# Kernel tuning notes

Hardware: AMD Instinct MI355X
Metric: run time of the kernel (lower is better)

The kernel has to match this reference:

```python
import jax, jax.numpy as jnp
import numpy as np

LOG2PI = 1.8378770664093453  # log(2*pi)


def _pixel_positions(d, h, w):
    # centered coordinates, stacked as (x, y, z) per the torch module
    z = jnp.arange(d, dtype=jnp.float32) - (d - 1) / 2.0
    y = jnp.arange(h, dtype=jnp.float32) - (h - 1) / 2.0
    x = jnp.arange(w, dtype=jnp.float32) - (w - 1) / 2.0
    zz = jnp.broadcast_to(z[:, None, None], (d, h, w))
    yy = jnp.broadcast_to(y[None, :, None], (d, h, w))
    xx = jnp.broadcast_to(x[None, None, :], (d, h, w))
    return jnp.stack([xx, yy, zz], axis=-1).reshape(-1, 3)  # (N, 3)


def setup_inputs() -> dict:
    key = jax.random.key(0)
    k0, k1, k2, k3, k4 = jax.random.split(key, 5)
    B, D = 512, 256
    d, h, w = 16, 64, 64
    scale = 1.0 / np.sqrt(D)
    return {
        "representation": jax.random.normal(k0, (B, D), dtype=jnp.float32),
        "mean_w": jax.random.normal(k1, (3, D), dtype=jnp.float32) * scale,
        "mean_b": jax.random.normal(k2, (3,), dtype=jnp.float32) * 0.1,
        "scale_w": jax.random.normal(k3, (6, D), dtype=jnp.float32) * scale,
        "scale_b": jax.random.normal(k4, (6,), dtype=jnp.float32) * 0.1,
        "pixel_positions": _pixel_positions(d, h, w),
    }


def reference(representation, mean_w, mean_b, scale_w, scale_b, pixel_positions):
    # linear heads
    means = representation @ mean_w.T + mean_b            # (B, 3)
    s_raw = representation @ scale_w.T + scale_b          # (B, 6)
    s = jax.nn.elu(s_raw) + 1.0                           # (B, 6)

    # FillScaleTriL with SoftplusTransform on the diagonal.
    # tril_indices(3,3) row-major order: (0,0),(1,0),(1,1),(2,0),(2,1),(2,2)
    l00 = jax.nn.softplus(s[:, 0])
    l10 = s[:, 1]
    l11 = jax.nn.softplus(s[:, 2])
    l20 = s[:, 3]
    l21 = s[:, 4]
    l22 = jax.nn.softplus(s[:, 5])

    # Mahalanobis term via analytic forward-substitution of L z = (x - mu)
    diff = pixel_positions[None, :, :] - means[:, None, :]  # (B, N, 3)
    z0 = diff[..., 0] / l00[:, None]
    z1 = (diff[..., 1] - l10[:, None] * z0) / l11[:, None]
    z2 = (diff[..., 2] - l20[:, None] * z0 - l21[:, None] * z1) / l22[:, None]
    maha = z0 * z0 + z1 * z1 + z2 * z2                     # (B, N)

    log_det = jnp.log(l00) + jnp.log(l11) + jnp.log(l22)   # (B,)
    log_probs = -0.5 * maha - 1.5 * LOG2PI - log_det[:, None]  # (B, N)

    # stable normalize over the pixel grid (matches torch code incl. eps)
    lp = log_probs - jnp.max(log_probs, axis=1, keepdims=True)
    p = jnp.exp(lp)
    return p / (jnp.sum(p, axis=1, keepdims=True) + 1e-10)
```

## Files before the change

kernel.cpp:

```cpp
#include <hip/hip_runtime.h>
#include <math.h>


#define LOG2PI_F 1.8378770664093453f

__device__ __forceinline__ float waveMax(float v) {
#pragma unroll
    for (int off = 32; off; off >>= 1) v = fmaxf(v, __shfl_xor(v, off, 64));
    return v;
}
__device__ __forceinline__ float waveSum(float v) {
#pragma unroll
    for (int off = 32; off; off >>= 1) v += __shfl_xor(v, off, 64);
    return v;
}

__global__ __launch_bounds__(1024, 4)
void mvn_profile_kernel(const float* __restrict__ rep,
                        const float* __restrict__ mean_w,
                        const float* __restrict__ mean_b,
                        const float* __restrict__ scale_w,
                        const float* __restrict__ scale_b,
                        float* __restrict__ out)
{
    const int b    = blockIdx.x;
    const int tid  = threadIdx.x;
    const int lane = tid & 63;
    const int wave = tid >> 6;

    __shared__ float s_dots[9];
    __shared__ float s_params[10];
    __shared__ float s_red[16];
    __shared__ float s_bcast;

    if (wave < 9) {
        const float4* r4 = (const float4*)(rep + (size_t)b * 256);
        const float*  wrow = (wave < 3) ? (mean_w + wave * 256)
                                        : (scale_w + (wave - 3) * 256);
        const float4* w4 = (const float4*)wrow;
        float4 a = r4[lane];
        float4 w = w4[lane];
        float d = a.x * w.x + a.y * w.y + a.z * w.z + a.w * w.w;
        d = waveSum(d);
        if (lane == 0) s_dots[wave] = d;
    }
    __syncthreads();

    if (tid == 0) {
        float mx = s_dots[0] + mean_b[0];
        float my = s_dots[1] + mean_b[1];
        float mz = s_dots[2] + mean_b[2];
        float s[6];
#pragma unroll
        for (int j = 0; j < 6; j++) {
            float x = s_dots[3 + j] + scale_b[j];
            s[j] = (x > 0.0f) ? (x + 1.0f) : (expm1f(x) + 1.0f);
        }
        float l00 = fmaxf(s[0], 0.0f) + log1pf(expf(-fabsf(s[0])));
        float l10 = s[1];
        float l11 = fmaxf(s[2], 0.0f) + log1pf(expf(-fabsf(s[2])));
        float l20 = s[3];
        float l21 = s[4];
        float l22 = fmaxf(s[5], 0.0f) + log1pf(expf(-fabsf(s[5])));
        s_params[0] = mx;
        s_params[1] = my;
        s_params[2] = mz;
        s_params[3] = 1.0f / l00;
        s_params[4] = l10;
        s_params[5] = 1.0f / l11;
        s_params[6] = l20;
        s_params[7] = l21;
        s_params[8] = 1.0f / l22;
        s_params[9] = -1.5f * LOG2PI_F - (logf(l00) + logf(l11) + logf(l22));
    }
    __syncthreads();

    const float mx  = s_params[0], my  = s_params[1], mz  = s_params[2];
    const float i00 = s_params[3], l10 = s_params[4], i11 = s_params[5];
    const float l20 = s_params[6], l21 = s_params[7], i22 = s_params[8];
    const float cb  = s_params[9];

    const float py = (float)(tid >> 4) - 31.5f;
    const float dy = py - my;

    float cc[4];
    float e2[4];
#pragma unroll
    for (int j = 0; j < 4; j++) {
        float px = (float)(((tid * 4) & 63) + j) - 31.5f;
        float dx = px - mx;
        float z0 = dx * i00;
        float z1 = (dy - l10 * z0) * i11;
        float c2 = mz + l20 * z0 + l21 * z1;
        e2[j] = c2 * i22;
        cc[j] = cb - 0.5f * (z0 * z0 + z1 * z1);
    }

    float lpv[64];
    float tmax = -INFINITY;
#pragma unroll
    for (int k = 0; k < 16; k++) {
        float t = ((float)k - 7.5f) * i22;
#pragma unroll
        for (int j = 0; j < 4; j++) {
            float z2 = t - e2[j];
            float lp = cc[j] - 0.5f * z2 * z2;
            lpv[k * 4 + j] = lp;
            tmax = fmaxf(tmax, lp);
        }
    }

    tmax = waveMax(tmax);
    if (lane == 0) s_red[wave] = tmax;
    __syncthreads();
    if (wave == 0) {
        float v = (lane < 16) ? s_red[lane] : -INFINITY;
        v = waveMax(v);
        if (lane == 0) s_bcast = v;
    }
    __syncthreads();
    const float m = s_bcast;

    float tsum = 0.0f;
#pragma unroll
    for (int i = 0; i < 64; i++) {
        float p = __expf(lpv[i] - m);
        lpv[i] = p;
        tsum += p;
    }
    tsum = waveSum(tsum);
    __syncthreads();
    if (lane == 0) s_red[wave] = tsum;
    __syncthreads();
    if (wave == 0) {
        float v = (lane < 16) ? s_red[lane] : 0.0f;
        v = waveSum(v);
        if (lane == 0) s_bcast = 1.0f / (v + 1e-10f);
    }
    __syncthreads();
    const float r = s_bcast;

    float* orow = out + (size_t)b * 65536 + (size_t)tid * 4;
#pragma unroll
    for (int k = 0; k < 16; k++) {
        float4 o;
        o.x = lpv[k * 4 + 0] * r;
        o.y = lpv[k * 4 + 1] * r;
        o.z = lpv[k * 4 + 2] * r;
        o.w = lpv[k * 4 + 3] * r;
        *(float4*)(orow + (size_t)k * 4096) = o;
    }
}

extern "C" void kernel_launch(void* const* d_in, const int* in_sizes, int n_in,
                              void* d_out, int out_size, void* d_ws, size_t ws_size,
                              hipStream_t stream) {
    const float* rep     = (const float*)d_in[0];
    const float* mean_w  = (const float*)d_in[1];
    const float* mean_b  = (const float*)d_in[2];
    const float* scale_w = (const float*)d_in[3];
    const float* scale_b = (const float*)d_in[4];
    float* out = (float*)d_out;

    const int B = in_sizes[0] / 256;
    hipLaunchKernelGGL(mvn_profile_kernel, dim3(B), dim3(1024), 0, stream,
                       rep, mean_w, mean_b, scale_w, scale_b, out);
}
```

Before: 156.5 us.

## Compute max analytically and recompute exp instead of holding 64 register values

Each thread's maximum over z is now found in closed form by rounding the continuous optimum to the nearest grid slice, so the 64-element log-prob array is no longer stored. The exponentials are computed twice, once for the sum and once at store time, which cuts register pressure and allows a higher occupancy hint (8 blocks per CU in launch bounds). Output stores use nontemporal hints and one redundant barrier is removed. This trades doubled exp work for fewer registers, and the analytic max depends on rintf rounding matching the true discrete argmax.

```diff
diff --git a/kernel.cpp b/kernel.cpp
--- a/kernel.cpp
+++ b/kernel.cpp
@@ -3,6 +3,8 @@
 
 
 #define LOG2PI_F 1.8378770664093453f
+
+typedef float fx4 __attribute__((ext_vector_type(4)));
 
 __device__ __forceinline__ float waveMax(float v) {
 #pragma unroll
@@ -15,7 +17,7 @@
     return v;
 }
 
-__global__ __launch_bounds__(1024, 4)
+__global__ __launch_bounds__(1024, 8)
 void mvn_profile_kernel(const float* __restrict__ rep,
                         const float* __restrict__ mean_w,
                         const float* __restrict__ mean_b,
@@ -31,7 +33,7 @@
     __shared__ float s_dots[9];
     __shared__ float s_params[10];
     __shared__ float s_red[16];
-    __shared__ float s_bcast;
+    __shared__ float s_bc[2];
 
     if (wave < 9) {
         const float4* r4 = (const float4*)(rep + (size_t)b * 256);
@@ -85,6 +87,7 @@
 
     float cc[4];
     float e2[4];
+    float tmax = -INFINITY;
 #pragma unroll
     for (int j = 0; j < 4; j++) {
         float px = (float)(((tid * 4) & 63) + j) - 31.5f;
@@ -94,20 +97,11 @@
         float c2 = mz + l20 * z0 + l21 * z1;
         e2[j] = c2 * i22;
         cc[j] = cb - 0.5f * (z0 * z0 + z1 * z1);
-    }
-
-    float lpv[64];
-    float tmax = -INFINITY;
-#pragma unroll
-    for (int k = 0; k < 16; k++) {
-        float t = ((float)k - 7.5f) * i22;
-#pragma unroll
-        for (int j = 0; j < 4; j++) {
-            float z2 = t - e2[j];
-            float lp = cc[j] - 0.5f * z2 * z2;
-            lpv[k * 4 + j] = lp;
-            tmax = fmaxf(tmax, lp);
-        }
+        float kf = rintf(c2 + 7.5f);
+        kf = fminf(fmaxf(kf, 0.0f), 15.0f);
+        float t  = (kf - 7.5f) * i22;
+        float z2 = t - e2[j];
+        tmax = fmaxf(tmax, cc[j] - 0.5f * (z2 * z2));
     }
 
     tmax = waveMax(tmax);
@@ -116,39 +110,50 @@
     if (wave == 0) {
         float v = (lane < 16) ? s_red[lane] : -INFINITY;
         v = waveMax(v);
-        if (lane == 0) s_bcast = v;
+        if (lane == 0) s_bc[0] = v;
     }
     __syncthreads();
-    const float m = s_bcast;
+    const float m = s_bc[0];
+
+    float ce[4];
+#pragma unroll
+    for (int j = 0; j < 4; j++) ce[j] = cc[j] - m;
 
     float tsum = 0.0f;
 #pragma unroll
-    for (int i = 0; i < 64; i++) {
-        float p = __expf(lpv[i] - m);
-        lpv[i] = p;
-        tsum += p;
+    for (int k = 0; k < 16; k++) {
+        float t = ((float)k - 7.5f) * i22;
+#pragma unroll
+        for (int j = 0; j < 4; j++) {
+            float z2 = t - e2[j];
+            tsum += __expf(ce[j] - 0.5f * (z2 * z2));
+        }
     }
     tsum = waveSum(tsum);
-    __syncthreads();
     if (lane == 0) s_red[wave] = tsum;
     __syncthreads();
     if (wave == 0) {
         float v = (lane < 16) ? s_red[lane] : 0.0f;
         v = waveSum(v);
-        if (lane == 0) s_bcast = 1.0f / (v + 1e-10f);
+        if (lane == 0) s_bc[1] = 1.0f / (v + 1e-10f);
     }
     __syncthreads();
-    const float r = s_bcast;
+    const float r = s_bc[1];
 
     float* orow = out + (size_t)b * 65536 + (size_t)tid * 4;
 #pragma unroll
     for (int k = 0; k < 16; k++) {
-        float4 o;
-        o.x = lpv[k * 4 + 0] * r;
-        o.y = lpv[k * 4 + 1] * r;
-        o.z = lpv[k * 4 + 2] * r;
-        o.w = lpv[k * 4 + 3] * r;
-        *(float4*)(orow + (size_t)k * 4096) = o;
+        float t = ((float)k - 7.5f) * i22;
+        float z20 = t - e2[0];
+        float z21 = t - e2[1];
+        float z22 = t - e2[2];
+        float z23 = t - e2[3];
+        fx4 o;
+        o.x = __expf(ce[0] - 0.5f * (z20 * z20)) * r;
+        o.y = __expf(ce[1] - 0.5f * (z21 * z21)) * r;
+        o.z = __expf(ce[2] - 0.5f * (z22 * z22)) * r;
+        o.w = __expf(ce[3] - 0.5f * (z23 * z23)) * r;
+        __builtin_nontemporal_store(o, (fx4*)(orow + (size_t)k * 4096));
     }
 }
 
```

Measured after the change: 189.8 us. 21.3% more time.
